# Optimization experiments

Hardware: AMD Instinct MI355X
Metric: run time of the kernel (lower is better)

Reference implementation:

```python
import jax, jax.numpy as jnp
import numpy as np

EMB, HID, NCH, CHK = 512, 1024, 16, 64   # hid_sz=1024, chunk_sz=64 -> 16 chunks
K, V = 5, 32000                           # n_mixtures, vocab
B, T = 8, 129
GATE = 4 * HID + 2 * NCH                  # i,f,o,g plus 2 master gates over chunks


def setup_inputs() -> dict:
    key = jax.random.key(0)
    ks = jax.random.split(key, 12)
    w = lambda k, shape: jax.random.normal(k, shape, jnp.float32) * 0.05
    return {
        "ys_token": jax.random.randint(ks[0], (B, T), 0, V),
        "emb": w(ks[1], (V, EMB)).at[0].set(0.0),  # padding_idx=0 row zeroed
        "Wx0": w(ks[2], (EMB, GATE)), "Wh0": w(ks[3], (HID, GATE)), "b0": jnp.zeros((GATE,), jnp.float32),
        "Wx1": w(ks[4], (HID, GATE)), "Wh1": w(ks[5], (HID, GATE)), "b1": jnp.zeros((GATE,), jnp.float32),
        "Wx2": w(ks[6], (HID, GATE)), "Wh2": w(ks[7], (HID, GATE)), "b2": jnp.zeros((GATE,), jnp.float32),
        "Wp": w(ks[8], (HID, K)), "bp": jnp.zeros((K,), jnp.float32),
        "Wl": w(ks[9], (HID, K * HID)), "bl": jnp.zeros((K * HID,), jnp.float32),
        "Wo": w(ks[10], (HID, V)), "bo": jnp.zeros((V,), jnp.float32),
    }


def _onlstm_cell(x, h, c, Wx, Wh, b):
    """One ON-LSTM step. Returns (h', c', master_forget_cumax)."""
    proj = x @ Wx + h @ Wh + b
    gates, masters = proj[:, : 4 * HID], proj[:, 4 * HID :]
    i, f, o, g = jnp.split(gates, 4, axis=-1)
    i, f, o = jax.nn.sigmoid(i), jax.nn.sigmoid(f), jax.nn.sigmoid(o)
    g = jnp.tanh(g)
    mf, mi = jnp.split(masters, 2, axis=-1)            # (B, NCH) each
    tf = jnp.cumsum(jax.nn.softmax(mf, -1), -1)        # master forget: cumax
    ti = 1.0 - jnp.cumsum(jax.nn.softmax(mi, -1), -1)  # master input: 1 - cumax
    tfe = jnp.repeat(tf, CHK, axis=-1)                 # expand chunks to HID
    tie = jnp.repeat(ti, CHK, axis=-1)
    w_ = tfe * tie
    c2 = (f * w_ + (tfe - w_)) * c + (i * w_ + (tie - w_)) * g
    h2 = o * jnp.tanh(c2)
    return h2, c2, tf


def reference(ys_token, emb, Wx0, Wh0, b0, Wx1, Wh1, b1, Wx2, Wh2, b2, Wp, bp, Wl, bl, Wo, bo):
    ys_in = ys_token[:, :-1]
    x = emb[ys_in]                                     # (B, T-1, EMB)
    z = jnp.zeros((B, HID), jnp.float32)

    def step(carry, xt):
        h0, c0, h1, c1, h2, c2 = carry
        h0, c0, _ = _onlstm_cell(xt, h0, c0, Wx0, Wh0, b0)
        h1, c1, tf1 = _onlstm_cell(h0, h1, c1, Wx1, Wh1, b1)  # s_layer = 1
        h2, c2, _ = _onlstm_cell(h1, h2, c2, Wx2, Wh2, b2)
        df = NCH - jnp.sum(tf1, -1)                    # expected split depth (B,)
        return (h0, c0, h1, c1, h2, c2), (h2, tf1, df)

    _, (outs, cf, df) = jax.lax.scan(step, (z, z, z, z, z, z), jnp.swapaxes(x, 0, 1))
    h = jnp.swapaxes(outs, 0, 1)                       # (B, L, HID)
    cf = jnp.swapaxes(cf, 0, 1)                        # (B, L, NCH)
    df = jnp.swapaxes(df, 0, 1)                        # (B, L)

    # Mixture-of-Softmaxes predictor
    log_prior = jax.nn.log_softmax(h @ Wp + bp, -1)    # (B, L, K)
    lat = jnp.tanh(h @ Wl + bl).reshape(B, T - 1, K, HID)
    mix = jax.nn.log_softmax(jnp.einsum("blkh,hv->blkv", lat, Wo) + bo, -1)
    logp = jax.nn.logsumexp(log_prior[..., None] + mix, axis=2)  # (B, L, V) log-probs

    gold = ys_token[:, 1:]
    mask = (gold != 0).astype(jnp.float32)
    nll = -jnp.take_along_axis(logp, gold[..., None], -1)[..., 0]
    per_seq = jnp.sum(nll * mask, 1) / (jnp.sum(mask, 1) + 1e-13)
    loss = jnp.mean(per_seq)
    pred = jnp.argmax(logp, -1)
    return loss, df, cf, pred
```

## Files before the change

### kernel.cpp

```cpp
#include <hip/hip_runtime.h>
#include <stdint.h>
#include <stddef.h>

#define TT   128
#define GATE 4128
#define VOC  32000
#define NWG  256

typedef float  f32x4 __attribute__((ext_vector_type(4)));
typedef short  bf16x8 __attribute__((ext_vector_type(8)));
typedef unsigned short u16x4 __attribute__((ext_vector_type(4)));

__device__ __forceinline__ float bf2f(ushort u){
  union { uint32_t i; float f; } c; c.i = ((uint32_t)u) << 16; return c.f;
}
__device__ __forceinline__ ushort f2bf(float x){
  uint32_t u = __builtin_bit_cast(uint32_t, x);
  uint32_t r = (u + 0x7fffu + ((u >> 16) & 1u)) >> 16;
  return (ushort)r;
}

__global__ void embed_kernel(const int* __restrict__ ys, const float* __restrict__ emb,
                             float* __restrict__ x){
  int r = blockIdx.x;
  int t = r >> 3, b = r & 7;
  int tok = ys[b*129 + t];
  f32x4 v = *(const f32x4*)&emb[(size_t)tok*512 + threadIdx.x*4];
  *(f32x4*)&x[(size_t)r*512 + threadIdx.x*4] = v;
}

__global__ void whT_kernel(const float* __restrict__ Wh, float* __restrict__ WhT){
  __shared__ float tile[32][33];
  int g0 = blockIdx.x*32, k0 = blockIdx.y*32;
  int tx = threadIdx.x, ty = threadIdx.y;
  for (int i = ty; i < 32; i += 8)
    tile[i][tx] = Wh[(size_t)(k0+i)*GATE + g0 + tx];
  __syncthreads();
  for (int i = ty; i < 32; i += 8)
    WhT[(size_t)(g0+i)*1024 + k0 + tx] = tile[tx][i];
}

__global__ void whmT_kernel(const float* __restrict__ Wh, float* __restrict__ WhmT){
  int idx = blockIdx.x*256 + threadIdx.x;
  int k = idx >> 5, c = idx & 31;
  WhmT[idx] = Wh[(size_t)k*GATE + 4096 + c];
}

__global__ __launch_bounds__(256) void wosplit_kernel(const float* __restrict__ Wo,
                                                      uint32_t* __restrict__ hi_img,
                                                      uint32_t* __restrict__ lo_img){
  __shared__ float tile[32][132];
  int ks = blockIdx.x, nt = blockIdx.y;
  int tid = threadIdx.x;
  for (int i = tid; i < 4096; i += 256)
    tile[i>>7][i&127] = Wo[(size_t)(ks*32 + (i>>7))*VOC + nt*128 + (i&127)];
  __syncthreads();
  size_t base = ((size_t)(nt*32 + ks)) << 11;
  for (int i = tid; i < 2048; i += 256){
    int p = i*4;
    int row = p >> 6, kgpos = (p >> 4) & 3, sub = (p >> 2) & 3;
    int kg = kgpos ^ ((row >> 1) & 3);
    int ke = kg*8 + 2*sub;
    float x0 = tile[ke][row], x1 = tile[ke+1][row];
    ushort h0 = f2bf(x0), h1 = f2bf(x1);
    ushort l0 = f2bf(x0 - bf2f(h0)), l1 = f2bf(x1 - bf2f(h1));
    hi_img[base + i] = (uint32_t)h0 | ((uint32_t)h1 << 16);
    lo_img[base + i] = (uint32_t)l0 | ((uint32_t)l1 << 16);
  }
}

template<int MODE>
__global__ __launch_bounds__(256) void gemm_f32_kernel(
    const float* __restrict__ X, const float* __restrict__ W, const float* __restrict__ bias,
    float* __restrict__ O1, ushort* __restrict__ O2, ushort* __restrict__ O3,
    int Kdim, int N)
{
  __shared__ float At[2][8][132];
  __shared__ float Bs[2][8][132];
  int tid = threadIdx.x;
  int n0 = blockIdx.x*128, r0 = blockIdx.y*128;
  int tx = tid & 15, ty = tid >> 4;
  int am = tid >> 1, akq = tid & 1;
  int bk = tid >> 5, bnc = tid & 31;
  float acc[8][8];
  #pragma unroll
  for (int i=0;i<8;i++)
    #pragma unroll
    for (int j=0;j<8;j++) acc[i][j]=0.f;
  {
    f32x4 av = *(const f32x4*)&X[(size_t)(r0+am)*Kdim + akq*4];
    At[0][akq*4+0][am]=av.x; At[0][akq*4+1][am]=av.y; At[0][akq*4+2][am]=av.z; At[0][akq*4+3][am]=av.w;
    int nb = n0 + bnc*4;
    f32x4 bv = {0.f,0.f,0.f,0.f};
    if (nb + 3 < N) bv = *(const f32x4*)&W[(size_t)bk*N + nb];
    *(f32x4*)&Bs[0][bk][bnc*4] = bv;
  }
  __syncthreads();
  int nk = Kdim >> 3;
  for (int ksb = 0; ksb < nk; ksb++){
    int cb = ksb & 1;
    if (ksb + 1 < nk){
      int k0 = (ksb+1)*8, bs = cb^1;
      f32x4 av = *(const f32x4*)&X[(size_t)(r0+am)*Kdim + k0 + akq*4];
      At[bs][akq*4+0][am]=av.x; At[bs][akq*4+1][am]=av.y; At[bs][akq*4+2][am]=av.z; At[bs][akq*4+3][am]=av.w;
      int nb = n0 + bnc*4;
      f32x4 bv = {0.f,0.f,0.f,0.f};
      if (nb + 3 < N) bv = *(const f32x4*)&W[(size_t)(k0+bk)*N + nb];
      *(f32x4*)&Bs[bs][bk][bnc*4] = bv;
    }
    #pragma unroll
    for (int k = 0; k < 8; k++){
      float a[8], b[8];
      *(f32x4*)&a[0] = *(const f32x4*)&At[cb][k][ty*8];
      *(f32x4*)&a[4] = *(const f32x4*)&At[cb][k][ty*8+4];
      *(f32x4*)&b[0] = *(const f32x4*)&Bs[cb][k][tx*8];
      *(f32x4*)&b[4] = *(const f32x4*)&Bs[cb][k][tx*8+4];
      #pragma unroll
      for (int i=0;i<8;i++)
        #pragma unroll
        for (int j=0;j<8;j++) acc[i][j] = fmaf(a[i], b[j], acc[i][j]);
    }
    __syncthreads();
  }
  #pragma unroll
  for (int i=0;i<8;i++){
    int r = r0 + ty*8 + i;
    #pragma unroll
    for (int j=0;j<8;j+=4){
      int n = n0 + tx*8 + j;
      if (n + 3 < N){
        f32x4 v;
        v.x = acc[i][j+0] + bias[n+0];
        v.y = acc[i][j+1] + bias[n+1];
        v.z = acc[i][j+2] + bias[n+2];
        v.w = acc[i][j+3] + bias[n+3];
        if (MODE >= 1){
          v.x = tanhf(v.x); v.y = tanhf(v.y); v.z = tanhf(v.z); v.w = tanhf(v.w);
        }
        *(f32x4*)&O1[(size_t)r*N + n] = v;
        if (MODE == 2){
          u16x4 h, l;
          #pragma unroll
          for (int q = 0; q < 4; q++){
            ushort hb = f2bf(v[q]);
            h[q] = hb;
            l[q] = f2bf(v[q] - bf2f(hb));
          }
          *(u16x4*)&O2[(size_t)r*N + n] = h;
          *(u16x4*)&O3[(size_t)r*N + n] = l;
        }
      }
    }
  }
}

__device__ __forceinline__ void gbar(int* flags, int* gen, int ep, int wg, int tid){
  if (wg == 0){
    if (tid == 0){
      __threadfence();
      __hip_atomic_store(&flags[0], ep, __ATOMIC_RELAXED, __HIP_MEMORY_SCOPE_AGENT);
    }
    if (tid < NWG){
      while (__hip_atomic_load(&flags[tid*16], __ATOMIC_RELAXED, __HIP_MEMORY_SCOPE_AGENT) < ep)
        __builtin_amdgcn_s_sleep(1);
    }
    __syncthreads();
    if (tid == 0){
      __threadfence();
      __hip_atomic_store(gen, ep, __ATOMIC_RELAXED, __HIP_MEMORY_SCOPE_AGENT);
      __threadfence();
    }
  } else {
    if (tid == 0){
      __threadfence();
      __hip_atomic_store(&flags[wg*16], ep, __ATOMIC_RELAXED, __HIP_MEMORY_SCOPE_AGENT);
      while (__hip_atomic_load(gen, __ATOMIC_RELAXED, __HIP_MEMORY_SCOPE_AGENT) < ep)
        __builtin_amdgcn_s_sleep(2);
      __threadfence();
    }
  }
}

__global__ __launch_bounds__(512) void scan_kernel(
    const float* __restrict__ A,
    const float* __restrict__ WhT,
    const float* __restrict__ WhmT,
    float* __restrict__ hbuf,
    float* __restrict__ H,
    float* __restrict__ cf_out, float* __restrict__ df_out,
    int* bar_flags, int* bar_gen, int* mflags, float* tfti)
{
  __shared__ __align__(16) float wls[1024*20];
  __shared__ __align__(16) float hls[1024*12];
  __shared__ __align__(16) float gpw[2][2][32][36];
  __shared__ float projg[8][16];
  __shared__ float cst[8][4];
  __shared__ float mpart[8][8][4];
  __shared__ float projmb[32];

  int tid = threadIdx.x, wg = blockIdx.x;
  int e0 = wg*4, chunk = wg >> 4;

  #pragma unroll
  for (int c = 0; c < 16; c++){
    int gcol = (c>>2)*1024 + e0 + (c&3);
    const float* src = WhT + (size_t)gcol*1024;
    for (int k = tid; k < 1024; k += 512)
      wls[k*20 + c] = src[k];
  }
  if (tid < 32) cst[tid & 7][tid >> 3] = 0.f;
  __syncthreads();

  int cq = tid >> 8;
  int bh = (tid >> 7) & 1;
  int kp = tid & 127;
  bool isM = (wg < 8);
  int mcg = tid & 7, mkp = tid >> 3;

  for (int t = 0; t < TT; t++){
    int rb = (t+1) & 1, wb = t & 1;
    float Ag = 0.f;
    if (tid < 128){
      int c = tid >> 3, b = tid & 7;
      Ag = A[(size_t)(t*8+b)*GATE + (c>>2)*1024 + e0 + (c&3)];
    }
    float Am = 0.f;
    if (isM && tid < 32) Am = A[(size_t)(t*8+wg)*GATE + 4096 + tid];

    {
      const f32x4* hb4 = (const f32x4*)&hbuf[rb*8192];
      #pragma unroll
      for (int s2 = 0; s2 < 4; s2++){
        int i4 = s2*512 + tid;
        f32x4 v = hb4[i4];
        int k = i4 >> 1, h2 = i4 & 1;
        *(f32x4*)&hls[k*12 + h2*4] = v;
      }
    }
    __syncthreads();

    if (isM){
      float macc[4] = {0.f,0.f,0.f,0.f};
      #pragma unroll
      for (int j = 0; j < 16; j++){
        int k = j*64 + mkp;
        f32x4 wm = *(const f32x4*)&WhmT[k*32 + mcg*4];
        float hv = hls[k*12 + wg];
        macc[0] += wm.x*hv; macc[1] += wm.y*hv; macc[2] += wm.z*hv; macc[3] += wm.w*hv;
      }
      #pragma unroll
      for (int off = 8; off < 64; off <<= 1){
        macc[0] += __shfl_xor(macc[0], off);
        macc[1] += __shfl_xor(macc[1], off);
        macc[2] += __shfl_xor(macc[2], off);
        macc[3] += __shfl_xor(macc[3], off);
      }
      if ((tid & 63) < 8){
        int wv = tid >> 6;
        mpart[wv][mcg][0] = macc[0]; mpart[wv][mcg][1] = macc[1];
        mpart[wv][mcg][2] = macc[2]; mpart[wv][mcg][3] = macc[3];
      }
      __syncthreads();
      if (tid < 32){
        float s = Am;
        #pragma unroll
        for (int wv = 0; wv < 8; wv++) s += mpart[wv][tid>>2][tid&3];
        projmb[tid] = s;
      }
      __syncthreads();
      if (tid < 32){
        int half = tid >> 4, j = tid & 15;
        float x = projmb[tid];
        float mx = x;
        #pragma unroll
        for (int o = 1; o < 16; o <<= 1) mx = fmaxf(mx, __shfl_xor(mx, o));
        float e = expf(x - mx);
        float ssum = e;
        #pragma unroll
        for (int o = 1; o < 16; o <<= 1) ssum += __shfl_xor(ssum, o);
        float sm = e / ssum;
        float c = sm;
        #pragma unroll
        for (int o = 1; o < 16; o <<= 1){
          float t2 = __shfl_up(c, o);
          if (j >= o) c += t2;
        }
        float outv = half ? (1.f - c) : c;
        tfti[half*128 + wg*16 + j] = outv;
        if (cf_out != nullptr && half == 0){
          cf_out[(wg*TT + t)*16 + j] = c;
          float ts = c;
          #pragma unroll
          for (int o = 1; o < 16; o <<= 1) ts += __shfl_xor(ts, o);
          if (j == 0) df_out[wg*TT + t] = 16.f - ts;
        }
      }
      __syncthreads();
      if (tid == 0){
        __threadfence();
        __hip_atomic_store(&mflags[wg*16], t+1, __ATOMIC_RELAXED, __HIP_MEMORY_SCOPE_AGENT);
      }
    }

    float acc[8][4];
    #pragma unroll
    for (int c = 0; c < 8; c++)
      #pragma unroll
      for (int b2 = 0; b2 < 4; b2++) acc[c][b2] = 0.f;
    #pragma unroll
    for (int j = 0; j < 8; j++){
      int k = j*128 + kp;
      float wa[8], hb[4];
      *(f32x4*)&wa[0] = *(const f32x4*)&wls[k*20 + cq*8];
      *(f32x4*)&wa[4] = *(const f32x4*)&wls[k*20 + cq*8 + 4];
      *(f32x4*)&hb[0] = *(const f32x4*)&hls[k*12 + bh*4];
      #pragma unroll
      for (int c = 0; c < 8; c++)
        #pragma unroll
        for (int b2 = 0; b2 < 4; b2++)
          acc[c][b2] = fmaf(wa[c], hb[b2], acc[c][b2]);
    }
    #pragma unroll
    for (int c = 0; c < 8; c++)
      #pragma unroll
      for (int b2 = 0; b2 < 4; b2++){
        float v = acc[c][b2];
        v += __shfl_xor(v, 1);
        v += __shfl_xor(v, 2);
        acc[c][b2] = v;
      }
    if ((kp & 3) == 0){
      int kg = kp >> 2;
      #pragma unroll
      for (int c = 0; c < 8; c++){
        f32x4 v4 = { acc[c][0], acc[c][1], acc[c][2], acc[c][3] };
        *(f32x4*)&gpw[cq][bh][kg][c*4] = v4;
      }
    }
    __syncthreads();
    if (tid < 128){
      int c = tid >> 3, b = tid & 7;
      float s = Ag;
      #pragma unroll
      for (int g = 0; g < 32; g++) s += gpw[c>>3][b>>2][g][(c&7)*4 + (b&3)];
      projg[b][c] = s;
    }
    if (tid < 8){
      while (__hip_atomic_load(&mflags[tid*16], __ATOMIC_RELAXED, __HIP_MEMORY_SCOPE_AGENT) < t+1)
        __builtin_amdgcn_s_sleep(1);
    }
    __syncthreads();
    if (tid < 32){
      int b = tid & 7, e = tid >> 3;
      float gi = projg[b][e], gf = projg[b][4+e], go = projg[b][8+e], gg = projg[b][12+e];
      float iv = 1.f/(1.f+expf(-gi)), fv = 1.f/(1.f+expf(-gf)), ov = 1.f/(1.f+expf(-go));
      float gv = tanhf(gg);
      float tf = __hip_atomic_load(&tfti[b*16 + chunk],       __ATOMIC_RELAXED, __HIP_MEMORY_SCOPE_AGENT);
      float ti = __hip_atomic_load(&tfti[128 + b*16 + chunk], __ATOMIC_RELAXED, __HIP_MEMORY_SCOPE_AGENT);
      float w  = tf*ti;
      float c2 = (fv*w + (tf - w))*cst[b][e] + (iv*w + (ti - w))*gv;
      cst[b][e] = c2;
      float h2 = ov * tanhf(c2);
      hbuf[wb*8192 + (e0+e)*8 + b] = h2;
      H[(size_t)(t*8+b)*1024 + e0 + e] = h2;
    }
    __syncthreads();
    gbar(bar_flags, bar_gen, t+1, wg, tid);
    __syncthreads();
  }
}

__device__ __forceinline__ void stageA_lds(const ushort* gsrc, char* ldsbase, int row0, int k0, int tid){
  int lane = tid & 63, wv = tid >> 6;
  #pragma unroll
  for (int s = 0; s < 2; s++){
    int p = wv*1024 + s*4096 + lane*16;
    int row = p >> 6;
    int kg  = (p >> 4) & 3;
    int kgs = kg ^ ((row >> 1) & 3);
    const ushort* ga = gsrc + (size_t)(row0 + row)*1024 + k0 + kgs*8;
    __builtin_amdgcn_global_load_lds(
        (const __attribute__((address_space(1))) void*)ga,
        (__attribute__((address_space(3))) void*)(ldsbase + wv*1024 + s*4096),
        16, 0, 0);
  }
}
__device__ __forceinline__ void stageB_pre(const char* img, char* lds, int nt, int ks, int tid){
  int lane = tid & 63, wv = tid >> 6;
  const char* base = img + (((size_t)(nt*32 + ks)) << 13);
  #pragma unroll
  for (int s = 0; s < 2; s++){
    int p = wv*1024 + s*4096 + lane*16;
    __builtin_amdgcn_global_load_lds(
        (const __attribute__((address_space(1))) void*)(base + p),
        (__attribute__((address_space(3))) void*)(lds + p),
        16, 0, 0);
  }
}
__device__ __forceinline__ void stageB_cv(const float* __restrict__ Wo, int n0, int k0, int tid,
                                          char* bhi, char* blo){
  int kp = tid & 15, g = tid >> 4;
  const float* src = Wo + (size_t)(k0 + 2*kp)*VOC + n0 + g*8;
  f32x4 v00 = *(const f32x4*)(src);
  f32x4 v01 = *(const f32x4*)(src + 4);
  f32x4 v10 = *(const f32x4*)(src + VOC);
  f32x4 v11 = *(const f32x4*)(src + VOC + 4);
  int kg = kp >> 2, sub = kp & 3;
  #pragma unroll
  for (int j = 0; j < 8; j++){
    float x0 = (j < 4) ? v00[j] : v01[j-4];
    float x1 = (j < 4) ? v10[j] : v11[j-4];
    ushort h0 = f2bf(x0), h1 = f2bf(x1);
    ushort l0 = f2bf(x0 - bf2f(h0)), l1 = f2bf(x1 - bf2f(h1));
    int n = g*8 + j;
    int byte = n*64 + ((kg ^ ((n >> 1) & 3)) << 4) + sub*4;
    *(uint32_t*)(bhi + byte) = (uint32_t)h0 | ((uint32_t)h1 << 16);
    *(uint32_t*)(blo + byte) = (uint32_t)l0 | ((uint32_t)l1 << 16);
  }
}
__device__ __forceinline__ bf16x8 rdfrag(const char* base, int row, int kg){
  int byte = row*64 + ((kg ^ ((row >> 1) & 3)) << 4);
  return *(const bf16x8*)(base + byte);
}

template<int PRE>
__global__ __launch_bounds__(256) void wo_gemm_kernel(
    const ushort* __restrict__ Ahi, const ushort* __restrict__ Alo,
    const float* __restrict__ Wo, const float* __restrict__ bo,
    const char* __restrict__ wohi_img, const char* __restrict__ wolo_img,
    float* __restrict__ S, float* __restrict__ partials, int rowbase)
{
  __shared__ __align__(16) char smem[66560];
  __shared__ float bo_s[128];
  __shared__ float redm[128][2], reds[128][2];
  int tid = threadIdx.x;
  int nt = blockIdx.x, mt = blockIdx.y;
  int n0 = nt*128, row0loc = mt*128, row0 = rowbase + row0loc;
  if (tid < 128) bo_s[tid] = bo[n0 + tid];
  f32x4 acc[4][4] = {};

  stageA_lds(Ahi, smem + 0,    row0, 0, tid);
  stageA_lds(Alo, smem + 8192, row0, 0, tid);
  if (PRE){
    stageB_pre(wohi_img, smem + 16384, nt, 0, tid);
    stageB_pre(wolo_img, smem + 24576, nt, 0, tid);
  } else {
    stageB_cv(Wo, n0, 0, tid, smem + 16384, smem + 24576);
  }
  __syncthreads();

  int lane = tid & 63, wv = tid >> 6;
  int wr = wv >> 1, wc = wv & 1;
  int rl = lane & 15, kgl = lane >> 4;
  for (int ks = 0; ks < 32; ks++){
    char* cb = smem + (ks & 1)*32768;
    if (ks + 1 < 32){
      char* nb2 = smem + ((ks+1) & 1)*32768;
      stageA_lds(Ahi, nb2,        row0, (ks+1)*32, tid);
      stageA_lds(Alo, nb2 + 8192, row0, (ks+1)*32, tid);
      if (PRE){
        stageB_pre(wohi_img, nb2 + 16384, nt, ks+1, tid);
        stageB_pre(wolo_img, nb2 + 24576, nt, ks+1, tid);
      } else {
        stageB_cv(Wo, n0, (ks+1)*32, tid, nb2 + 16384, nb2 + 24576);
      }
    }
    bf16x8 ah[4], al[4], bh[4], bl2[4];
    #pragma unroll
    for (int m = 0; m < 4; m++){
      int row = wr*64 + m*16 + rl;
      ah[m] = rdfrag(cb,        row, kgl);
      al[m] = rdfrag(cb + 8192, row, kgl);
    }
    #pragma unroll
    for (int n = 0; n < 4; n++){
      int rw = wc*64 + n*16 + rl;
      bh[n]  = rdfrag(cb + 16384, rw, kgl);
      bl2[n] = rdfrag(cb + 24576, rw, kgl);
    }
    #pragma unroll
    for (int m = 0; m < 4; m++)
      #pragma unroll
      for (int n = 0; n < 4; n++){
        acc[m][n] = __builtin_amdgcn_mfma_f32_16x16x32_bf16(ah[m], bh[n],  acc[m][n], 0,0,0);
        acc[m][n] = __builtin_amdgcn_mfma_f32_16x16x32_bf16(ah[m], bl2[n], acc[m][n], 0,0,0);
        acc[m][n] = __builtin_amdgcn_mfma_f32_16x16x32_bf16(al[m], bh[n],  acc[m][n], 0,0,0);
      }
    __syncthreads();
  }

  float* st = (float*)smem;
  #pragma unroll
  for (int m = 0; m < 4; m++){
    int rb = wr*64 + m*16 + (lane >> 4)*4;
    #pragma unroll
    for (int n = 0; n < 4; n++){
      int col = wc*64 + n*16 + rl;
      #pragma unroll
      for (int j = 0; j < 4; j++)
        st[(rb + j)*130 + col] = acc[m][n][j];
    }
  }
  __syncthreads();
  int row = tid >> 1, half = tid & 1;
  float lmax = -1e30f;
  for (int jc = 0; jc < 64; jc += 4){
    f32x4 v;
    #pragma unroll
    for (int j = 0; j < 4; j++){
      float x = st[row*130 + half*64 + jc + j] + bo_s[half*64 + jc + j];
      st[row*130 + half*64 + jc + j] = x;
      v[j] = x;
      lmax = fmaxf(lmax, x);
    }
    *(f32x4*)&S[(size_t)(row0loc + row)*VOC + n0 + half*64 + jc] = v;
  }
  redm[row][half] = lmax;
  __syncthreads();
  float rm = fmaxf(redm[row][0], redm[row][1]);
  float lsum = 0.f;
  for (int jc = 0; jc < 64; jc++)
    lsum += expf(st[row*130 + half*64 + jc] - rm);
  reds[row][half] = lsum;
  __syncthreads();
  if (half == 0){
    float2 pr; pr.x = rm; pr.y = reds[row][0] + reds[row][1];
    *(float2*)&partials[((size_t)(row0loc + row)*250 + nt)*2] = pr;
  }
}

__device__ __forceinline__ float cand_q(const float* __restrict__ srow, int v,
                                        float l0, float l1, float l2, float l3, float l4){
  float t0 = l0 + srow[v];
  float t1 = l1 + srow[VOC   + v];
  float t2 = l2 + srow[2*VOC + v];
  float t3 = l3 + srow[3*VOC + v];
  float t4 = l4 + srow[4*VOC + v];
  float m = fmaxf(fmaxf(fmaxf(t0,t1),fmaxf(t2,t3)),t4);
  return m + logf(expf(t0-m)+expf(t1-m)+expf(t2-m)+expf(t3-m)+expf(t4-m));
}
__global__ __launch_bounds__(256) void cand_kernel(
    const float* __restrict__ S, const double* __restrict__ lp,
    const float* __restrict__ partials, double* __restrict__ Zd,
    int* __restrict__ cand, int rbase)
{
  int g = blockIdx.x; int r = rbase + g; int tid = threadIdx.x;
  __shared__ float lpk[5];
  __shared__ double zk[5];
  __shared__ float rq[256]; __shared__ int rv[256];
  __shared__ double rd[256];
  __shared__ int cnt; __shared__ int list[64];
  if (tid == 0) cnt = 0;
  for (int k = 0; k < 5; k++){
    size_t lrow = (size_t)(g*5 + k);
    float m = -1e30f;
    for (int t2 = tid; t2 < 250; t2 += 256) m = fmaxf(m, partials[(lrow*250 + t2)*2]);
    rq[tid] = m; __syncthreads();
    for (int s = 128; s; s >>= 1){ if (tid < s) rq[tid] = fmaxf(rq[tid], rq[tid+s]); __syncthreads(); }
    float M = rq[0]; __syncthreads();
    double ssum = 0.0;
    for (int t2 = tid; t2 < 250; t2 += 256){
      float pm = partials[(lrow*250 + t2)*2];
      float se = partials[(lrow*250 + t2)*2 + 1];
      ssum += exp((double)pm - (double)M)*(double)se;
    }
    rd[tid] = ssum; __syncthreads();
    for (int s = 128; s; s >>= 1){ if (tid < s) rd[tid] += rd[tid+s]; __syncthreads(); }
    if (tid == 0){
      double z = (double)M + log(rd[0]);
      zk[k] = z;
      Zd[lrow] = z;
    }
    __syncthreads();
  }
  if (tid < 5) lpk[tid] = (float)(lp[r*5 + tid] - zk[tid]);
  __syncthreads();
  float l0 = lpk[0], l1 = lpk[1], l2 = lpk[2], l3 = lpk[3], l4 = lpk[4];
  const float* srow = S + (size_t)(g*5)*VOC;
  float bq = -1e30f; int bv = 0;
  for (int v = tid; v < VOC; v += 256){
    float q = cand_q(srow, v, l0,l1,l2,l3,l4);
    if (q > bq){ bq = q; bv = v; }
  }
  rq[tid] = bq; rv[tid] = bv; __syncthreads();
  for (int s = 128; s > 0; s >>= 1){
    if (tid < s){
      if (rq[tid+s] > rq[tid] || (rq[tid+s] == rq[tid] && rv[tid+s] < rv[tid])){
        rq[tid] = rq[tid+s]; rv[tid] = rv[tid+s];
      }
    }
    __syncthreads();
  }
  float M = rq[0]; int argv = rv[0];
  for (int v = tid; v < VOC; v += 256){
    float q = cand_q(srow, v, l0,l1,l2,l3,l4);
    if (q >= M - 0.02f && v != argv){
      int ix = atomicAdd(&cnt, 1);
      if (ix < 63) list[ix] = v;
    }
  }
  __syncthreads();
  int nc = cnt < 63 ? cnt : 63;
  if (tid == 0){ cand[r*66] = nc + 1; cand[r*66 + 1] = argv; }
  if (tid < nc) cand[r*66 + 2 + tid] = list[tid];
}

__global__ __launch_bounds__(256) void refine_kernel(
    const float* __restrict__ lat, const float* __restrict__ Wo, const float* __restrict__ bo,
    const double* __restrict__ lp, const double* __restrict__ Z,
    const int* __restrict__ cand, const int* __restrict__ ys,
    float* __restrict__ nll, float* __restrict__ pred_out)
{
  int r = blockIdx.x, tid = threadIdx.x;
  int b = r & 7, l = r >> 3;
  int nc = cand[r*66];
  if (nc < 0) nc = 0;
  if (nc > 64) nc = 64;
  __shared__ double dred[5][4];
  __shared__ double bestval; __shared__ int bestv;
  if (tid == 0){ bestval = -1e300; bestv = 0; }
  __syncthreads();
  int gold = ys[b*129 + l + 1];
  for (int ci = 0; ci <= nc; ci++){
    int v = (ci < nc) ? cand[r*66 + 1 + ci] : gold;
    double p0=0,p1=0,p2=0,p3=0,p4=0;
    for (int h = tid; h < 1024; h += 256){
      double w = (double)Wo[(size_t)h*VOC + v];
      p0 += (double)lat[((size_t)r*5+0)*1024 + h]*w;
      p1 += (double)lat[((size_t)r*5+1)*1024 + h]*w;
      p2 += (double)lat[((size_t)r*5+2)*1024 + h]*w;
      p3 += (double)lat[((size_t)r*5+3)*1024 + h]*w;
      p4 += (double)lat[((size_t)r*5+4)*1024 + h]*w;
    }
    #pragma unroll
    for (int off = 32; off; off >>= 1){
      p0 += __shfl_down(p0, off); p1 += __shfl_down(p1, off);
      p2 += __shfl_down(p2, off); p3 += __shfl_down(p3, off);
      p4 += __shfl_down(p4, off);
    }
    if ((tid & 63) == 0){
      int w = tid >> 6;
      dred[0][w]=p0; dred[1][w]=p1; dred[2][w]=p2; dred[3][w]=p3; dred[4][w]=p4;
    }
    __syncthreads();
    if (tid == 0){
      double bv = (double)bo[v];
      double tk[5]; double mx = -1e300;
      #pragma unroll
      for (int k = 0; k < 5; k++){
        double sk = dred[k][0]+dred[k][1]+dred[k][2]+dred[k][3] + bv;
        tk[k] = (lp[r*5+k] - Z[r*5+k]) + sk;
        mx = tk[k] > mx ? tk[k] : mx;
      }
      double q = mx + log(exp(tk[0]-mx)+exp(tk[1]-mx)+exp(tk[2]-mx)+exp(tk[3]-mx)+exp(tk[4]-mx));
      if (ci < nc){
        if (q > bestval || (q == bestval && v < bestv)){ bestval = q; bestv = v; }
      } else {
        nll[r] = (float)(-q);
      }
    }
    __syncthreads();
  }
  if (tid == 0) pred_out[b*TT + l] = (float)bestv;
}

__global__ __launch_bounds__(64) void prior_kernel(
    const float* __restrict__ H2, const float* __restrict__ Wp, const float* __restrict__ bp,
    double* __restrict__ lp)
{
  int r = blockIdx.x, tid = threadIdx.x;
  double p0=0,p1=0,p2=0,p3=0,p4=0;
  for (int h = tid; h < 1024; h += 64){
    double x = (double)H2[(size_t)r*1024 + h];
    const float* w = &Wp[h*5];
    p0 += x*(double)w[0]; p1 += x*(double)w[1]; p2 += x*(double)w[2];
    p3 += x*(double)w[3]; p4 += x*(double)w[4];
  }
  #pragma unroll
  for (int off = 32; off; off >>= 1){
    p0 += __shfl_down(p0, off); p1 += __shfl_down(p1, off);
    p2 += __shfl_down(p2, off); p3 += __shfl_down(p3, off);
    p4 += __shfl_down(p4, off);
  }
  if (tid == 0){
    double lg[5] = { p0+(double)bp[0], p1+(double)bp[1], p2+(double)bp[2], p3+(double)bp[3], p4+(double)bp[4] };
    double mx = lg[0];
    #pragma unroll
    for (int k = 1; k < 5; k++) mx = lg[k] > mx ? lg[k] : mx;
    double s = 0;
    #pragma unroll
    for (int k = 0; k < 5; k++) s += exp(lg[k]-mx);
    double lse = mx + log(s);
    #pragma unroll
    for (int k = 0; k < 5; k++) lp[r*5+k] = lg[k] - lse;
  }
}

__global__ void loss_kernel(const float* __restrict__ nll, const int* __restrict__ ys,
                            float* __restrict__ out){
  int tid = threadIdx.x;
  __shared__ float ps[8];
  if (tid < 8){
    float s = 0.f, ms = 0.f;
    for (int l = 0; l < TT; l++){
      int gold = ys[tid*129 + l + 1];
      float m = (gold != 0) ? 1.f : 0.f;
      s  += nll[l*8 + tid]*m;
      ms += m;
    }
    ps[tid] = s/(ms + 1e-13f);
  }
  __syncthreads();
  if (tid == 0){
    float t = 0.f;
    for (int b = 0; b < 8; b++) t += ps[b];
    out[0] = t/8.f;
  }
}

extern "C" void kernel_launch(void* const* d_in, const int* in_sizes, int n_in,
                              void* d_out, int out_size, void* d_ws, size_t ws_size,
                              hipStream_t stream)
{
  (void)in_sizes; (void)n_in; (void)out_size;
  const int*   ys  = (const int*)  d_in[0];
  const float* emb = (const float*)d_in[1];
  const float* Wx0 = (const float*)d_in[2];
  const float* Wh0 = (const float*)d_in[3];
  const float* b0  = (const float*)d_in[4];
  const float* Wx1 = (const float*)d_in[5];
  const float* Wh1 = (const float*)d_in[6];
  const float* b1  = (const float*)d_in[7];
  const float* Wx2 = (const float*)d_in[8];
  const float* Wh2 = (const float*)d_in[9];
  const float* b2  = (const float*)d_in[10];
  const float* Wp  = (const float*)d_in[11];
  const float* bp  = (const float*)d_in[12];
  const float* Wl  = (const float*)d_in[13];
  const float* bl  = (const float*)d_in[14];
  const float* Wo  = (const float*)d_in[15];
  const float* bo  = (const float*)d_in[16];
  float* out = (float*)d_out;

  char* ws = (char*)d_ws;
  size_t off = 0;
  auto alloc = [&](size_t bytes){ size_t o = off; off += (bytes + 255) & ~(size_t)255; return o; };
  size_t o_hbuf = alloc(2*8192*4);
  size_t o_bars = alloc(3*(NWG*16 + 16)*sizeof(int));
  size_t o_mfl  = alloc(3*8*16*sizeof(int));
  size_t zero_bytes = off;
  size_t o_tfti = alloc(256*4);
  size_t o_x    = alloc((size_t)1024*512*4);
  size_t o_whT  = alloc((size_t)GATE*1024*4);
  size_t o_whmT = alloc((size_t)1024*32*4);
  size_t o_A    = alloc((size_t)1024*GATE*4);
  size_t o_H0   = alloc((size_t)1024*1024*4);
  size_t o_H1   = alloc((size_t)1024*1024*4);
  size_t o_H2   = alloc((size_t)1024*1024*4);
  size_t o_lp   = alloc((size_t)1024*5*8);
  size_t o_latf = alloc((size_t)1024*5120*4);
  size_t o_lath = alloc((size_t)5120*1024*2);
  size_t o_latl = alloc((size_t)5120*1024*2);
  size_t o_Z    = alloc((size_t)5120*8);
  size_t o_cand = alloc((size_t)1024*66*4);
  size_t o_nll  = alloc((size_t)1024*4);
  size_t base   = off;

  const size_t woimg = (size_t)250*32*8192;
  auto need = [&](int ch, int pre){
    return base + (pre ? 2*((woimg + 255) & ~(size_t)255) : 0)
                + (((size_t)ch*250*2*4 + 255) & ~(size_t)255)
                + (((size_t)ch*VOC*4 + 255) & ~(size_t)255);
  };
  int PRE, CH;
  if      (need(1280,1) <= ws_size){ PRE=1; CH=1280; }
  else if (need(640, 1) <= ws_size){ PRE=1; CH=640;  }
  else if (need(1280,0) <= ws_size){ PRE=0; CH=1280; }
  else                              { PRE=0; CH=640;  }
  size_t o_wohi = 0, o_wolo = 0;
  if (PRE){ o_wohi = alloc(woimg); o_wolo = alloc(woimg); }
  size_t o_part = alloc((size_t)CH*250*2*4);
  size_t o_s    = alloc((size_t)CH*VOC*4);
  (void)o_s;

  float*  hbuf  = (float*) (ws + o_hbuf);
  int*    bars  = (int*)   (ws + o_bars);
  int*    mfl   = (int*)   (ws + o_mfl);
  float*  tfti  = (float*) (ws + o_tfti);
  float*  xbuf  = (float*) (ws + o_x);
  float*  whT   = (float*) (ws + o_whT);
  float*  whmT  = (float*) (ws + o_whmT);
  float*  Abuf  = (float*) (ws + o_A);
  float*  H0    = (float*) (ws + o_H0);
  float*  H1    = (float*) (ws + o_H1);
  float*  H2    = (float*) (ws + o_H2);
  double* lpbuf = (double*)(ws + o_lp);
  float*  latf  = (float*) (ws + o_latf);
  ushort* lath  = (ushort*)(ws + o_lath);
  ushort* latl  = (ushort*)(ws + o_latl);
  double* Zbuf  = (double*)(ws + o_Z);
  int*    candb = (int*)   (ws + o_cand);
  float*  nllb  = (float*) (ws + o_nll);
  char*   wohi  = ws + o_wohi;
  char*   wolo  = ws + o_wolo;
  float*  partb = (float*) (ws + o_part);
  float*  Sbuf  = (float*) (ws + o_s);

  int perl = NWG*16 + 16;
  int* flags0 = bars;             int* gen0 = flags0 + NWG*16;
  int* flags1 = bars + perl;      int* gen1 = flags1 + NWG*16;
  int* flags2 = bars + 2*perl;    int* gen2 = flags2 + NWG*16;
  int* mfl0 = mfl;  int* mfl1 = mfl + 8*16;  int* mfl2 = mfl + 16*16;

  hipMemsetAsync(d_ws, 0, zero_bytes, stream);
  embed_kernel<<<1024, 128, 0, stream>>>(ys, emb, xbuf);
  if (PRE)
    wosplit_kernel<<<dim3(32,250), 256, 0, stream>>>(Wo, (uint32_t*)wohi, (uint32_t*)wolo);

  gemm_f32_kernel<0><<<dim3(33,8), 256, 0, stream>>>(xbuf, Wx0, b0, Abuf, nullptr, nullptr, 512, GATE);
  whT_kernel<<<dim3(129,32), dim3(32,8), 0, stream>>>(Wh0, whT);
  whmT_kernel<<<128, 256, 0, stream>>>(Wh0, whmT);
  scan_kernel<<<NWG, 512, 0, stream>>>(Abuf, whT, whmT, hbuf, H0, nullptr, nullptr,
                                       flags0, gen0, mfl0, tfti);
  gemm_f32_kernel<0><<<dim3(33,8), 256, 0, stream>>>(H0, Wx1, b1, Abuf, nullptr, nullptr, 1024, GATE);
  whT_kernel<<<dim3(129,32), dim3(32,8), 0, stream>>>(Wh1, whT);
  whmT_kernel<<<128, 256, 0, stream>>>(Wh1, whmT);
  hipMemsetAsync(hbuf, 0, 2*8192*4, stream);
  scan_kernel<<<NWG, 512, 0, stream>>>(Abuf, whT, whmT, hbuf, H1, out + 1025, out + 1,
                                       flags1, gen1, mfl1, tfti);
  gemm_f32_kernel<0><<<dim3(33,8), 256, 0, stream>>>(H1, Wx2, b2, Abuf, nullptr, nullptr, 1024, GATE);
  whT_kernel<<<dim3(129,32), dim3(32,8), 0, stream>>>(Wh2, whT);
  whmT_kernel<<<128, 256, 0, stream>>>(Wh2, whmT);
  hipMemsetAsync(hbuf, 0, 2*8192*4, stream);
  scan_kernel<<<NWG, 512, 0, stream>>>(Abuf, whT, whmT, hbuf, H2, nullptr, nullptr,
                                       flags2, gen2, mfl2, tfti);

  prior_kernel<<<1024, 64, 0, stream>>>(H2, Wp, bp, lpbuf);
  gemm_f32_kernel<2><<<dim3(40,8), 256, 0, stream>>>(H2, Wl, bl, latf, lath, latl, 1024, 5120);

  int nchunks = 5120 / CH;
  for (int c = 0; c < nchunks; c++){
    if (PRE)
      wo_gemm_kernel<1><<<dim3(250, CH/128), 256, 0, stream>>>(lath, latl, Wo, bo, wohi, wolo, Sbuf, partb, c*CH);
    else
      wo_gemm_kernel<0><<<dim3(250, CH/128), 256, 0, stream>>>(lath, latl, Wo, bo, nullptr, nullptr, Sbuf, partb, c*CH);
    cand_kernel<<<CH/5, 256, 0, stream>>>(Sbuf, lpbuf, partb, Zbuf + c*CH, candb, c*(CH/5));
  }
  refine_kernel<<<1024, 256, 0, stream>>>(latf, Wo, bo, lpbuf, Zbuf, candb, ys, nllb, out + 17409);
  loss_kernel<<<1, 64, 0, stream>>>(nllb, ys, out);
}
```

Baseline: 8.965 ms.

## Route input-projection and latent GEMMs through split-bf16 MFMA kernels

```diff
diff --git a/kernel.cpp b/kernel.cpp
--- a/kernel.cpp
+++ b/kernel.cpp
@@ -44,6 +44,33 @@
   int idx = blockIdx.x*256 + threadIdx.x;
   int k = idx >> 5, c = idx & 31;
   WhmT[idx] = Wh[(size_t)k*GATE + 4096 + c];
+}
+
+__global__ __launch_bounds__(256) void wsplit_kernel(const float* __restrict__ W,
+                                                     uint32_t* __restrict__ hi_img,
+                                                     uint32_t* __restrict__ lo_img,
+                                                     int K, int N, int KS){
+  __shared__ float tile[32][132];
+  int ks = blockIdx.x, nt = blockIdx.y;
+  int tid = threadIdx.x;
+  for (int i = tid; i < 4096; i += 256){
+    int n = nt*128 + (i & 127);
+    int k = ks*32 + (i >> 7);
+    tile[i>>7][i&127] = (n < N) ? W[(size_t)k*N + n] : 0.f;
+  }
+  __syncthreads();
+  size_t base = ((size_t)(nt*KS + ks)) << 11;
+  for (int i = tid; i < 2048; i += 256){
+    int p = i*4;
+    int row = p >> 6, kgpos = (p >> 4) & 3, sub = (p >> 2) & 3;
+    int kg = kgpos ^ ((row >> 1) & 3);
+    int ke = kg*8 + 2*sub;
+    float x0 = tile[ke][row], x1 = tile[ke+1][row];
+    ushort h0 = f2bf(x0), h1 = f2bf(x1);
+    ushort l0 = f2bf(x0 - bf2f(h0)), l1 = f2bf(x1 - bf2f(h1));
+    hi_img[base + i] = (uint32_t)h0 | ((uint32_t)h1 << 16);
+    lo_img[base + i] = (uint32_t)l0 | ((uint32_t)l1 << 16);
+  }
 }
 
 __global__ __launch_bounds__(256) void wosplit_kernel(const float* __restrict__ Wo,
@@ -67,6 +94,21 @@
     hi_img[base + i] = (uint32_t)h0 | ((uint32_t)h1 << 16);
     lo_img[base + i] = (uint32_t)l0 | ((uint32_t)l1 << 16);
   }
+}
+
+__global__ __launch_bounds__(256) void xsplit_kernel(const float* __restrict__ X,
+                                                     ushort* __restrict__ hi, ushort* __restrict__ lo){
+  int i = (blockIdx.x*256 + threadIdx.x)*4;
+  f32x4 v = *(const f32x4*)&X[i];
+  u16x4 h, l;
+  #pragma unroll
+  for (int j = 0; j < 4; j++){
+    ushort hb = f2bf(v[j]);
+    h[j] = hb;
+    l[j] = f2bf(v[j] - bf2f(hb));
+  }
+  *(u16x4*)&hi[i] = h;
+  *(u16x4*)&lo[i] = l;
 }
 
 template<int MODE>
@@ -149,6 +191,137 @@
           *(u16x4*)&O2[(size_t)r*N + n] = h;
           *(u16x4*)&O3[(size_t)r*N + n] = l;
         }
+      }
+    }
+  }
+}
+
+__device__ __forceinline__ void stageA_ldsK(const ushort* gsrc, char* ldsbase, int row0, int k0,
+                                            int tid, int Kdim){
+  int lane = tid & 63, wv = tid >> 6;
+  #pragma unroll
+  for (int s = 0; s < 2; s++){
+    int p = wv*1024 + s*4096 + lane*16;
+    int row = p >> 6;
+    int kg  = (p >> 4) & 3;
+    int kgs = kg ^ ((row >> 1) & 3);
+    const ushort* ga = gsrc + (size_t)(row0 + row)*Kdim + k0 + kgs*8;
+    __builtin_amdgcn_global_load_lds(
+        (const __attribute__((address_space(1))) void*)ga,
+        (__attribute__((address_space(3))) void*)(ldsbase + wv*1024 + s*4096),
+        16, 0, 0);
+  }
+}
+__device__ __forceinline__ void stageB_img(const char* img, char* lds, int nt, int ks, int KS, int tid){
+  int lane = tid & 63, wv = tid >> 6;
+  const char* base = img + (((size_t)(nt*KS + ks)) << 13);
+  #pragma unroll
+  for (int s = 0; s < 2; s++){
+    int p = wv*1024 + s*4096 + lane*16;
+    __builtin_amdgcn_global_load_lds(
+        (const __attribute__((address_space(1))) void*)(base + p),
+        (__attribute__((address_space(3))) void*)(lds + p),
+        16, 0, 0);
+  }
+}
+__device__ __forceinline__ bf16x8 rdfrag(const char* base, int row, int kg){
+  int byte = row*64 + ((kg ^ ((row >> 1) & 3)) << 4);
+  return *(const bf16x8*)(base + byte);
+}
+
+template<int MODE>
+__global__ __launch_bounds__(256) void xw_gemm_kernel(
+    const ushort* __restrict__ Xhi, const ushort* __restrict__ Xlo, int Kdim, int KS,
+    const char* __restrict__ whi_img, const char* __restrict__ wlo_img,
+    const float* __restrict__ bias, int N,
+    float* __restrict__ O1, ushort* __restrict__ O2, ushort* __restrict__ O3)
+{
+  __shared__ __align__(16) char smem[66560];
+  __shared__ float bo_s[128];
+  int tid = threadIdx.x;
+  int nt = blockIdx.x, mt = blockIdx.y;
+  int n0 = nt*128, row0 = mt*128;
+  if (tid < 128) bo_s[tid] = (n0 + tid < N) ? bias[n0 + tid] : 0.f;
+  f32x4 acc[4][4] = {};
+
+  stageA_ldsK(Xhi, smem + 0,    row0, 0, tid, Kdim);
+  stageA_ldsK(Xlo, smem + 8192, row0, 0, tid, Kdim);
+  stageB_img(whi_img, smem + 16384, nt, 0, KS, tid);
+  stageB_img(wlo_img, smem + 24576, nt, 0, KS, tid);
+  __syncthreads();
+
+  int lane = tid & 63, wv = tid >> 6;
+  int wr = wv >> 1, wc = wv & 1;
+  int rl = lane & 15, kgl = lane >> 4;
+  for (int ks = 0; ks < KS; ks++){
+    char* cb = smem + (ks & 1)*32768;
+    if (ks + 1 < KS){
+      char* nb2 = smem + ((ks+1) & 1)*32768;
+      stageA_ldsK(Xhi, nb2,        row0, (ks+1)*32, tid, Kdim);
+      stageA_ldsK(Xlo, nb2 + 8192, row0, (ks+1)*32, tid, Kdim);
+      stageB_img(whi_img, nb2 + 16384, nt, ks+1, KS, tid);
+      stageB_img(wlo_img, nb2 + 24576, nt, ks+1, KS, tid);
+    }
+    bf16x8 ah[4], al[4], bh[4], bl2[4];
+    #pragma unroll
+    for (int m = 0; m < 4; m++){
+      int row = wr*64 + m*16 + rl;
+      ah[m] = rdfrag(cb,        row, kgl);
+      al[m] = rdfrag(cb + 8192, row, kgl);
+    }
+    #pragma unroll
+    for (int n = 0; n < 4; n++){
+      int rw = wc*64 + n*16 + rl;
+      bh[n]  = rdfrag(cb + 16384, rw, kgl);
+      bl2[n] = rdfrag(cb + 24576, rw, kgl);
+    }
+    #pragma unroll
+    for (int m = 0; m < 4; m++)
+      #pragma unroll
+      for (int n = 0; n < 4; n++){
+        acc[m][n] = __builtin_amdgcn_mfma_f32_16x16x32_bf16(ah[m], bh[n],  acc[m][n], 0,0,0);
+        acc[m][n] = __builtin_amdgcn_mfma_f32_16x16x32_bf16(ah[m], bl2[n], acc[m][n], 0,0,0);
+        acc[m][n] = __builtin_amdgcn_mfma_f32_16x16x32_bf16(al[m], bh[n],  acc[m][n], 0,0,0);
+      }
+    __syncthreads();
+  }
+
+  float* st = (float*)smem;
+  #pragma unroll
+  for (int m = 0; m < 4; m++){
+    int rb = wr*64 + m*16 + (lane >> 4)*4;
+    #pragma unroll
+    for (int n = 0; n < 4; n++){
+      int col = wc*64 + n*16 + rl;
+      #pragma unroll
+      for (int j = 0; j < 4; j++)
+        st[(rb + j)*130 + col] = acc[m][n][j];
+    }
+  }
+  __syncthreads();
+  int row = tid >> 1, half = tid & 1;
+  int r = row0 + row;
+  for (int jc = 0; jc < 64; jc += 4){
+    int n = n0 + half*64 + jc;
+    if (n + 3 < N){
+      f32x4 v;
+      #pragma unroll
+      for (int j = 0; j < 4; j++){
+        float x = st[row*130 + half*64 + jc + j] + bo_s[half*64 + jc + j];
+        if (MODE == 2) x = tanhf(x);
+        v[j] = x;
+      }
+      *(f32x4*)&O1[(size_t)r*N + n] = v;
+      if (MODE == 2){
+        u16x4 h, l;
+        #pragma unroll
+        for (int q = 0; q < 4; q++){
+          ushort hb = f2bf(v[q]);
+          h[q] = hb;
+          l[q] = f2bf(v[q] - bf2f(hb));
+        }
+        *(u16x4*)&O2[(size_t)r*N + n] = h;
+        *(u16x4*)&O3[(size_t)r*N + n] = l;
       }
     }
   }
@@ -370,33 +543,6 @@
   }
 }
 
-__device__ __forceinline__ void stageA_lds(const ushort* gsrc, char* ldsbase, int row0, int k0, int tid){
-  int lane = tid & 63, wv = tid >> 6;
-  #pragma unroll
-  for (int s = 0; s < 2; s++){
-    int p = wv*1024 + s*4096 + lane*16;
-    int row = p >> 6;
-    int kg  = (p >> 4) & 3;
-    int kgs = kg ^ ((row >> 1) & 3);
-    const ushort* ga = gsrc + (size_t)(row0 + row)*1024 + k0 + kgs*8;
-    __builtin_amdgcn_global_load_lds(
-        (const __attribute__((address_space(1))) void*)ga,
-        (__attribute__((address_space(3))) void*)(ldsbase + wv*1024 + s*4096),
-        16, 0, 0);
-  }
-}
-__device__ __forceinline__ void stageB_pre(const char* img, char* lds, int nt, int ks, int tid){
-  int lane = tid & 63, wv = tid >> 6;
-  const char* base = img + (((size_t)(nt*32 + ks)) << 13);
-  #pragma unroll
-  for (int s = 0; s < 2; s++){
-    int p = wv*1024 + s*4096 + lane*16;
-    __builtin_amdgcn_global_load_lds(
-        (const __attribute__((address_space(1))) void*)(base + p),
-        (__attribute__((address_space(3))) void*)(lds + p),
-        16, 0, 0);
-  }
-}
 __device__ __forceinline__ void stageB_cv(const float* __restrict__ Wo, int n0, int k0, int tid,
                                           char* bhi, char* blo){
   int kp = tid & 15, g = tid >> 4;
@@ -418,10 +564,6 @@
     *(uint32_t*)(blo + byte) = (uint32_t)l0 | ((uint32_t)l1 << 16);
   }
 }
-__device__ __forceinline__ bf16x8 rdfrag(const char* base, int row, int kg){
-  int byte = row*64 + ((kg ^ ((row >> 1) & 3)) << 4);
-  return *(const bf16x8*)(base + byte);
-}
 
 template<int PRE>
 __global__ __launch_bounds__(256) void wo_gemm_kernel(
@@ -439,11 +581,11 @@
   if (tid < 128) bo_s[tid] = bo[n0 + tid];
   f32x4 acc[4][4] = {};
 
-  stageA_lds(Ahi, smem + 0,    row0, 0, tid);
-  stageA_lds(Alo, smem + 8192, row0, 0, tid);
+  stageA_ldsK(Ahi, smem + 0,    row0, 0, tid, 1024);
+  stageA_ldsK(Alo, smem + 8192, row0, 0, tid, 1024);
   if (PRE){
-    stageB_pre(wohi_img, smem + 16384, nt, 0, tid);
-    stageB_pre(wolo_img, smem + 24576, nt, 0, tid);
+    stageB_img(wohi_img, smem + 16384, nt, 0, 32, tid);
+    stageB_img(wolo_img, smem + 24576, nt, 0, 32, tid);
   } else {
     stageB_cv(Wo, n0, 0, tid, smem + 16384, smem + 24576);
   }
@@ -456,11 +598,11 @@
     char* cb = smem + (ks & 1)*32768;
     if (ks + 1 < 32){
       char* nb2 = smem + ((ks+1) & 1)*32768;
-      stageA_lds(Ahi, nb2,        row0, (ks+1)*32, tid);
-      stageA_lds(Alo, nb2 + 8192, row0, (ks+1)*32, tid);
+      stageA_ldsK(Ahi, nb2,        row0, (ks+1)*32, tid, 1024);
+      stageA_ldsK(Alo, nb2 + 8192, row0, (ks+1)*32, tid, 1024);
       if (PRE){
-        stageB_pre(wohi_img, nb2 + 16384, nt, ks+1, tid);
-        stageB_pre(wolo_img, nb2 + 24576, nt, ks+1, tid);
+        stageB_img(wohi_img, nb2 + 16384, nt, ks+1, 32, tid);
+        stageB_img(wolo_img, nb2 + 24576, nt, ks+1, 32, tid);
       } else {
         stageB_cv(Wo, n0, (ks+1)*32, tid, nb2 + 16384, nb2 + 24576);
       }
@@ -766,19 +908,34 @@
   size_t o_nll  = alloc((size_t)1024*4);
   size_t base   = off;
 
-  const size_t woimg = (size_t)250*32*8192;
-  auto need = [&](int ch, int pre){
+  const size_t woimg  = (size_t)250*32*8192;
+  const size_t wx0img = (size_t)33*16*8192;
+  const size_t wx1img = (size_t)33*32*8192;
+  const size_t wlimg  = (size_t)40*32*8192;
+  const size_t xsz    = (size_t)1024*1024*2;
+  const size_t imgtot = 2*(wx0img + 2*wx1img + wlimg + xsz) + 6*256;
+  auto need = [&](int ch, int pre, int img){
     return base + (pre ? 2*((woimg + 255) & ~(size_t)255) : 0)
+                + (img ? imgtot + 4096 : 0)
                 + (((size_t)ch*250*2*4 + 255) & ~(size_t)255)
                 + (((size_t)ch*VOC*4 + 255) & ~(size_t)255);
   };
-  int PRE, CH;
-  if      (need(1280,1) <= ws_size){ PRE=1; CH=1280; }
-  else if (need(640, 1) <= ws_size){ PRE=1; CH=640;  }
-  else if (need(1280,0) <= ws_size){ PRE=0; CH=1280; }
-  else                              { PRE=0; CH=640;  }
+  int PRE, CH, IMG;
+  if      (need(1280,1,1) <= ws_size){ PRE=1; CH=1280; IMG=1; }
+  else if (need(1280,1,0) <= ws_size){ PRE=1; CH=1280; IMG=0; }
+  else if (need(640, 1,0) <= ws_size){ PRE=1; CH=640;  IMG=0; }
+  else if (need(1280,0,0) <= ws_size){ PRE=0; CH=1280; IMG=0; }
+  else                                { PRE=0; CH=640;  IMG=0; }
   size_t o_wohi = 0, o_wolo = 0;
   if (PRE){ o_wohi = alloc(woimg); o_wolo = alloc(woimg); }
+  size_t o_wx0h=0,o_wx0l=0,o_wx1h=0,o_wx1l=0,o_wx2h=0,o_wx2l=0,o_wlh=0,o_wll=0,o_xh=0,o_xl=0;
+  if (IMG){
+    o_wx0h = alloc(wx0img); o_wx0l = alloc(wx0img);
+    o_wx1h = alloc(wx1img); o_wx1l = alloc(wx1img);
+    o_wx2h = alloc(wx1img); o_wx2l = alloc(wx1img);
+    o_wlh  = alloc(wlimg);  o_wll  = alloc(wlimg);
+    o_xh   = alloc(xsz);    o_xl   = alloc(xsz);
+  }
   size_t o_part = alloc((size_t)CH*250*2*4);
   size_t o_s    = alloc((size_t)CH*VOC*4);
   (void)o_s;
@@ -805,6 +962,8 @@
   char*   wolo  = ws + o_wolo;
   float*  partb = (float*) (ws + o_part);
   float*  Sbuf  = (float*) (ws + o_s);
+  ushort* xhi   = (ushort*)(ws + o_xh);
+  ushort* xlo   = (ushort*)(ws + o_xl);
 
   int perl = NWG*16 + 16;
   int* flags0 = bars;             int* gen0 = flags0 + NWG*16;
@@ -816,19 +975,43 @@
   embed_kernel<<<1024, 128, 0, stream>>>(ys, emb, xbuf);
   if (PRE)
     wosplit_kernel<<<dim3(32,250), 256, 0, stream>>>(Wo, (uint32_t*)wohi, (uint32_t*)wolo);
-
-  gemm_f32_kernel<0><<<dim3(33,8), 256, 0, stream>>>(xbuf, Wx0, b0, Abuf, nullptr, nullptr, 512, GATE);
+  if (IMG){
+    wsplit_kernel<<<dim3(16,33), 256, 0, stream>>>(Wx0, (uint32_t*)(ws+o_wx0h), (uint32_t*)(ws+o_wx0l), 512, GATE, 16);
+    wsplit_kernel<<<dim3(32,33), 256, 0, stream>>>(Wx1, (uint32_t*)(ws+o_wx1h), (uint32_t*)(ws+o_wx1l), 1024, GATE, 32);
+    wsplit_kernel<<<dim3(32,33), 256, 0, stream>>>(Wx2, (uint32_t*)(ws+o_wx2h), (uint32_t*)(ws+o_wx2l), 1024, GATE, 32);
+    wsplit_kernel<<<dim3(32,40), 256, 0, stream>>>(Wl,  (uint32_t*)(ws+o_wlh),  (uint32_t*)(ws+o_wll),  1024, 5120, 32);
+  }
+
+  if (IMG){
+    xsplit_kernel<<<512, 256, 0, stream>>>(xbuf, xhi, xlo);
+    xw_gemm_kernel<0><<<dim3(33,8), 256, 0, stream>>>(xhi, xlo, 512, 16,
+        ws+o_wx0h, ws+o_wx0l, b0, GATE, Abuf, nullptr, nullptr);
+  } else {
+    gemm_f32_kernel<0><<<dim3(33,8), 256, 0, stream>>>(xbuf, Wx0, b0, Abuf, nullptr, nullptr, 512, GATE);
+  }
   whT_kernel<<<dim3(129,32), dim3(32,8), 0, stream>>>(Wh0, whT);
   whmT_kernel<<<128, 256, 0, stream>>>(Wh0, whmT);
   scan_kernel<<<NWG, 512, 0, stream>>>(Abuf, whT, whmT, hbuf, H0, nullptr, nullptr,
                                        flags0, gen0, mfl0, tfti);
-  gemm_f32_kernel<0><<<dim3(33,8), 256, 0, stream>>>(H0, Wx1, b1, Abuf, nullptr, nullptr, 1024, GATE);
+  if (IMG){
+    xsplit_kernel<<<1024, 256, 0, stream>>>(H0, xhi, xlo);
+    xw_gemm_kernel<0><<<dim3(33,8), 256, 0, stream>>>(xhi, xlo, 1024, 32,
+        ws+o_wx1h, ws+o_wx1l, b1, GATE, Abuf, nullptr, nullptr);
+  } else {
+    gemm_f32_kernel<0><<<dim3(33,8), 256, 0, stream>>>(H0, Wx1, b1, Abuf, nullptr, nullptr, 1024, GATE);
+  }
   whT_kernel<<<dim3(129,32), dim3(32,8), 0, stream>>>(Wh1, whT);
   whmT_kernel<<<128, 256, 0, stream>>>(Wh1, whmT);
   hipMemsetAsync(hbuf, 0, 2*8192*4, stream);
   scan_kernel<<<NWG, 512, 0, stream>>>(Abuf, whT, whmT, hbuf, H1, out + 1025, out + 1,
                                        flags1, gen1, mfl1, tfti);
-  gemm_f32_kernel<0><<<dim3(33,8), 256, 0, stream>>>(H1, Wx2, b2, Abuf, nullptr, nullptr, 1024, GATE);
+  if (IMG){
+    xsplit_kernel<<<1024, 256, 0, stream>>>(H1, xhi, xlo);
+    xw_gemm_kernel<0><<<dim3(33,8), 256, 0, stream>>>(xhi, xlo, 1024, 32,
+        ws+o_wx2h, ws+o_wx2l, b2, GATE, Abuf, nullptr, nullptr);
+  } else {
+    gemm_f32_kernel<0><<<dim3(33,8), 256, 0, stream>>>(H1, Wx2, b2, Abuf, nullptr, nullptr, 1024, GATE);
+  }
   whT_kernel<<<dim3(129,32), dim3(32,8), 0, stream>>>(Wh2, whT);
   whmT_kernel<<<128, 256, 0, stream>>>(Wh2, whmT);
   hipMemsetAsync(hbuf, 0, 2*8192*4, stream);
@@ -836,7 +1019,13 @@
                                        flags2, gen2, mfl2, tfti);
 
   prior_kernel<<<1024, 64, 0, stream>>>(H2, Wp, bp, lpbuf);
-  gemm_f32_kernel<2><<<dim3(40,8), 256, 0, stream>>>(H2, Wl, bl, latf, lath, latl, 1024, 5120);
+  if (IMG){
+    xsplit_kernel<<<1024, 256, 0, stream>>>(H2, xhi, xlo);
+    xw_gemm_kernel<2><<<dim3(40,8), 256, 0, stream>>>(xhi, xlo, 1024, 32,
+        ws+o_wlh, ws+o_wll, bl, 5120, latf, lath, latl);
+  } else {
+    gemm_f32_kernel<2><<<dim3(40,8), 256, 0, stream>>>(H2, Wl, bl, latf, lath, latl, 1024, 5120);
+  }
 
   int nchunks = 5120 / CH;
   for (int c = 0; c < nchunks; c++){
```

Result: faster. 8.627 ms (median of 2 runs) (-3.8%).
